# Kernel tuning notes

Measured on AMD Instinct MI355X. Metric: run time of the kernel, lower is better.

The kernel has to match this reference:

```python
import jax, jax.numpy as jnp
import numpy as np

# Qwen2 MoE MLP layer: top-k router -> token dispatch -> grouped SwiGLU MLP -> weighted combine.
S, B, H = 2048, 1, 1024      # seq, batch, hidden
E, K, F = 8, 2, 1408         # num_experts, top_k, moe_intermediate (fc1 emits 2*F for SwiGLU)

def setup_inputs() -> dict:
    key = jax.random.key(0)
    k1, k2, k3, k4 = jax.random.split(key, 4)
    return {
        "hidden_states": jax.random.normal(k1, (S, B, H), jnp.float32),
        "router_weight": jax.random.normal(k2, (H, E), jnp.float32) * 0.02,
        "w1": jax.random.normal(k3, (E, H, 2 * F), jnp.float32) * 0.02,  # grouped fc1 (gate|up)
        "w2": jax.random.normal(k4, (E, F, H), jnp.float32) * 0.02,      # grouped fc2
    }

def reference(hidden_states, router_weight, w1, w2):
    s, b, h = hidden_states.shape
    x = hidden_states.reshape(-1, h)                      # [T, H], T = S*B
    logits = x @ router_weight                            # [T, E]
    probs = jax.nn.softmax(logits, axis=-1)
    _, topk_idx = jax.lax.top_k(probs, K)                 # token -> top-k expert ids
    routing_map = jax.nn.one_hot(topk_idx, E, dtype=probs.dtype).sum(axis=1)  # [T, E] 0/1 mask
    local_probs = probs * routing_map                     # combine weights, zero off-topk
    # Grouped SwiGLU MLP. The torch module permutes tokens to expert groups and runs
    # grouped GEMMs; with static shapes the equivalent math is dense-per-expert with
    # the routing mask folded into the combine weights (identical output).
    y = jnp.einsum('th,ehf->tef', x, w1)                  # [T, E, 2F]
    y1, y2 = jnp.split(y, 2, axis=-1)
    g = jax.nn.silu(y1) * y2                              # swiglu, [T, E, F]
    o = jnp.einsum('tef,efh->teh', g, w2)                 # [T, E, H]
    out = jnp.einsum('teh,te->th', o, local_probs)        # unpermute + prob-weighted combine
    return out.reshape(s, b, h)
```

## Files before the change

### kernel.cpp

```cpp
#include <hip/hip_runtime.h>
#include <hip/hip_bf16.h>
#include <stdint.h>

#define T_TOK 2048
#define HD    1024
#define NE    8
#define FD    1408
#define F2D   2816
#define HP    1056
#define OP    1056

#define BM 128
#define BK 32
#define MAXMT 40
#define MAXSLOTS 5120
#define FC1_NT 22
#define FC2_NT 16
#define FC1_NWG (FC1_NT * MAXMT)
#define FC2_NWG (FC2_NT * MAXMT)
#define FC1_CHUNK 110
#define FC2_CHUNK 80

typedef __attribute__((ext_vector_type(8))) short bf16x8;
typedef __attribute__((ext_vector_type(4))) float f32x4;
typedef __attribute__((ext_vector_type(2))) int i32x2;

__device__ __forceinline__ unsigned short f2bf(float f) {
  unsigned int u = __float_as_uint(f);
  u += 0x7FFFu + ((u >> 16) & 1u);
  return (unsigned short)(u >> 16);
}

#define GLL16(gp, lp) __builtin_amdgcn_global_load_lds( \
    (const __attribute__((address_space(1))) void*)(gp), \
    (__attribute__((address_space(3))) void*)(lp), 16, 0, 0)

#define LDS_OFF(p) ((unsigned)(uintptr_t)(__attribute__((address_space(3))) const unsigned short*)(p))

__device__ __forceinline__ void tr_issue(unsigned a, i32x2& lo, i32x2& hi) {
  asm volatile("ds_read_b64_tr_b16 %0, %2\n\t"
               "ds_read_b64_tr_b16 %1, %2 offset:512"
               : "=&v"(lo), "=&v"(hi)
               : "v"(a)
               : "memory");
}
__device__ __forceinline__ bf16x8 tr_pack(i32x2 lo, i32x2 hi) {
  union { i32x2 v; short s[4]; } a, b;
  a.v = lo; b.v = hi;
  bf16x8 f;
  f[0] = a.s[0]; f[1] = a.s[1]; f[2] = a.s[2]; f[3] = a.s[3];
  f[4] = b.s[0]; f[5] = b.s[1]; f[6] = b.s[2]; f[7] = b.s[3];
  return f;
}

__global__ __launch_bounds__(256) void k_router(
    const float* __restrict__ x, const float* __restrict__ rw,
    unsigned short* __restrict__ xbf, int* __restrict__ ctrl,
    int* __restrict__ tok_e, float* __restrict__ tok_p)
{
  const int lane = threadIdx.x & 63;
  const int t = blockIdx.x * 4 + (threadIdx.x >> 6);
  const float* xr = x + (size_t)t * HD;

  float part[8];
#pragma unroll
  for (int e = 0; e < 8; ++e) part[e] = 0.f;

#pragma unroll
  for (int i = 0; i < 16; ++i) {
    const int h = i * 64 + lane;
    const float xv = xr[h];
    xbf[(size_t)t * HP + h] = f2bf(xv);
    const float4* rwr = reinterpret_cast<const float4*>(rw + (size_t)h * 8);
    float4 a = rwr[0], bb = rwr[1];
    part[0] += xv * a.x; part[1] += xv * a.y; part[2] += xv * a.z; part[3] += xv * a.w;
    part[4] += xv * bb.x; part[5] += xv * bb.y; part[6] += xv * bb.z; part[7] += xv * bb.w;
  }
#pragma unroll
  for (int e = 0; e < 8; ++e) {
    float v = part[e];
#pragma unroll
    for (int d = 32; d; d >>= 1) v += __shfl_xor(v, d, 64);
    part[e] = v;
  }
  float m = part[0];
#pragma unroll
  for (int e = 1; e < 8; ++e) m = fmaxf(m, part[e]);
  float p[8], s = 0.f;
#pragma unroll
  for (int e = 0; e < 8; ++e) { p[e] = __expf(part[e] - m); s += p[e]; }
  const float inv = 1.f / s;
#pragma unroll
  for (int e = 0; e < 8; ++e) p[e] *= inv;

  int e0 = 0; float p0 = p[0];
#pragma unroll
  for (int e = 1; e < 8; ++e) if (p[e] > p0) { p0 = p[e]; e0 = e; }
  int e1 = -1; float p1 = -1.f;
#pragma unroll
  for (int e = 0; e < 8; ++e) if (e != e0 && p[e] > p1) { p1 = p[e]; e1 = e; }

  if (lane == 0) {
    tok_e[t * 2 + 0] = e0; tok_e[t * 2 + 1] = e1;
    tok_p[t * 2 + 0] = p0; tok_p[t * 2 + 1] = p1;
    atomicAdd(&ctrl[e0], 1);
    atomicAdd(&ctrl[e1], 1);
  }
}

__global__ __launch_bounds__(256) void k_offsets(
    int* __restrict__ ctrl, const int* __restrict__ tok_e,
    const float* __restrict__ tok_p, int* __restrict__ stok,
    float* __restrict__ sp, int* __restrict__ tslot,
    int* __restrict__ widmt1, int* __restrict__ widmt2)
{
  __shared__ int soff[8], scnt[8], sFirst[8], sNmt[8], sTake[8], sCur[8];
  __shared__ int sSpill;
  if (threadIdx.x == 0) {
    int o = 0, nm = 0, spill = 0;
    for (int e = 0; e < 8; ++e) {
      ctrl[16 + e] = o; soff[e] = o; scnt[e] = ctrl[e]; sCur[e] = 0;
      const int n = ctrl[e];
      const int nmt = (n + BM - 1) / BM;
      sFirst[e] = nm; sNmt[e] = nmt; sTake[e] = nmt < 5 ? nmt : 5;
      if (nmt > 5) spill = 1;
      for (int j = 0; j < nmt; ++j) { ctrl[24 + nm] = e; ctrl[64 + nm] = o + j * BM; ++nm; }
      o += nmt * BM;
    }
    for (int i = nm; i < MAXMT; ++i) ctrl[24 + i] = -1;
    sSpill = spill;
  }
  __syncthreads();
  for (int i = threadIdx.x; i < FC1_NWG; i += 256) {
    const int e = i / FC1_CHUNK, r = i % FC1_CHUNK;
    const int j = r / FC1_NT, n = r % FC1_NT;
    widmt1[i] = (j < sTake[e]) ? (sFirst[e] + j) * 32 + n : -1;
  }
  for (int i = threadIdx.x; i < FC2_NWG; i += 256) {
    const int e = i / FC2_CHUNK, r = i % FC2_CHUNK;
    const int j = r / FC2_NT, n = r % FC2_NT;
    widmt2[i] = (j < sTake[e]) ? (sFirst[e] + j) * 32 + n : -1;
  }
  __syncthreads();
  if (sSpill && threadIdx.x == 0) {
    int cur = 0;
    for (int e = 0; e < 8; ++e)
      for (int j = 5; j < sNmt[e]; ++j)
        for (int n = 0; n < FC1_NT; ++n) {
          while (widmt1[cur] != -1) ++cur;
          widmt1[cur] = (sFirst[e] + j) * 32 + n;
        }
    cur = 0;
    for (int e = 0; e < 8; ++e)
      for (int j = 5; j < sNmt[e]; ++j)
        for (int n = 0; n < FC2_NT; ++n) {
          while (widmt2[cur] != -1) ++cur;
          widmt2[cur] = (sFirst[e] + j) * 32 + n;
        }
  }
  for (int e = 0; e < 8; ++e) {
    const int n = scnt[e], o = soff[e];
    const int padEnd = (n + BM - 1) / BM * BM;
    for (int j = n + (int)threadIdx.x; j < padEnd; j += 256) {
      stok[o + j] = 0; sp[o + j] = 0.f;
    }
  }
  for (int i = threadIdx.x; i < T_TOK; i += 256) {
#pragma unroll
    for (int k = 0; k < 2; ++k) {
      const int e = tok_e[i * 2 + k];
      const int pos = atomicAdd(&sCur[e], 1);
      const int slot = soff[e] + pos;
      stok[slot] = i; sp[slot] = tok_p[i * 2 + k];
      tslot[i * 2 + k] = slot;
    }
  }
}

__global__ __launch_bounds__(256) void k_fc1(
    const unsigned short* __restrict__ xbf,
    const float* __restrict__ w1,
    const int* __restrict__ ctrl,
    const int* __restrict__ stok,
    const float* __restrict__ sp,
    const int* __restrict__ widmt1,
    unsigned short* __restrict__ g)
{
  const int bid = blockIdx.x;
  const int wid = (bid & 7) * FC1_CHUNK + (bid >> 3);
  const int packed = widmt1[wid];
  if (packed < 0) return;
  const int mt = packed >> 5;
  const int e = ctrl[24 + mt];
  const int rowbase = ctrl[64 + mt];
  const int n0 = (packed & 31) * 64;

  __shared__ unsigned short sA[3][BM * BK];
  __shared__ unsigned short sB1[3][64 * BK];
  __shared__ unsigned short sB2[3][64 * BK];

  const int tid = threadIdx.x;
  const int lane = tid & 63;
  const int wave = tid >> 6;
  const int wm = wave >> 1, wn = wave & 1;

  const int schunk = (lane & 3) ^ ((lane >> 3) & 3);
  const unsigned short* aSrc[2];
#pragma unroll
  for (int t4 = 0; t4 < 2; ++t4) {
    const int row = (t4 * 4 + wave) * 16 + (lane >> 2);
    const int tok = stok[rowbase + row];
    aSrc[t4] = xbf + (size_t)tok * HP + schunk * 8;
  }

  const int kdec = wave * 8 + ((lane >> 5) << 2) + ((lane >> 1) & 3);
  const int ndec = ((lane >> 3) & 3) * 16 + (lane & 1) * 8;
  const float* b1SrcF = w1 + ((size_t)e * HD + kdec) * F2D + n0 + ndec;
  const float* b2SrcF = b1SrcF + FD;

  const int c = lane >> 4;
  int aoff[4];
#pragma unroll
  for (int m = 0; m < 4; ++m) {
    const int row = wm * 64 + m * 16 + (lane & 15);
    aoff[m] = row * 32 + ((c ^ ((row >> 1) & 3)) << 3);
  }
  const unsigned trlane = (lane & 15) * 8 + (lane >> 4) * 1024;
  unsigned trb[2];
#pragma unroll
  for (int n = 0; n < 2; ++n) trb[n] = trlane + (wn * 2 + n) * 128;
  const unsigned b1base = LDS_OFF(&sB1[0][0]);
  const unsigned b2base = LDS_OFF(&sB2[0][0]);

  const f32x4 zero = {0.f, 0.f, 0.f, 0.f};
  f32x4 acc1[4][2], acc2[4][2];
#pragma unroll
  for (int m = 0; m < 4; ++m)
#pragma unroll
    for (int n = 0; n < 2; ++n) { acc1[m][n] = zero; acc2[m][n] = zero; }

  float b1r0[8], b2r0[8], b1r1[8], b2r1[8];

#define FC1_BLOAD(KT, R1, R2) do {                                  \
    const float* _p1 = b1SrcF + (size_t)(KT) * BK * F2D;            \
    const float* _p2 = b2SrcF + (size_t)(KT) * BK * F2D;            \
    *(float4*)&R1[0] = *(const float4*)_p1;                         \
    *(float4*)&R1[4] = *(const float4*)(_p1 + 4);                   \
    *(float4*)&R2[0] = *(const float4*)_p2;                         \
    *(float4*)&R2[4] = *(const float4*)(_p2 + 4);                   \
  } while (0)

#define FC1_BWRITE(BUF, R1, R2) do {                                \
    unsigned _a0,_a1,_a2,_a3,_c0,_c1,_c2,_c3;                       \
    asm("v_cvt_pk_bf16_f32 %0, %1, %2" : "=v"(_a0) : "v"(R1[0]), "v"(R1[1])); \
    asm("v_cvt_pk_bf16_f32 %0, %1, %2" : "=v"(_a1) : "v"(R1[2]), "v"(R1[3])); \
    asm("v_cvt_pk_bf16_f32 %0, %1, %2" : "=v"(_a2) : "v"(R1[4]), "v"(R1[5])); \
    asm("v_cvt_pk_bf16_f32 %0, %1, %2" : "=v"(_a3) : "v"(R1[6]), "v"(R1[7])); \
    asm("v_cvt_pk_bf16_f32 %0, %1, %2" : "=v"(_c0) : "v"(R2[0]), "v"(R2[1])); \
    asm("v_cvt_pk_bf16_f32 %0, %1, %2" : "=v"(_c1) : "v"(R2[2]), "v"(R2[3])); \
    asm("v_cvt_pk_bf16_f32 %0, %1, %2" : "=v"(_c2) : "v"(R2[4]), "v"(R2[5])); \
    asm("v_cvt_pk_bf16_f32 %0, %1, %2" : "=v"(_c3) : "v"(R2[6]), "v"(R2[7])); \
    uint4 _u1 = make_uint4(_a0,_a1,_a2,_a3);                        \
    uint4 _u2 = make_uint4(_c0,_c1,_c2,_c3);                        \
    *(uint4*)&sB1[BUF][wave * 512 + lane * 8] = _u1;                \
    *(uint4*)&sB2[BUF][wave * 512 + lane * 8] = _u2;                \
  } while (0)

#define FC1_ASTAGE(BUF, KT) do {                                    \
    for (int _t4 = 0; _t4 < 2; ++_t4)                               \
      GLL16(aSrc[_t4] + (size_t)(KT) * BK, &sA[BUF][(_t4 * 4 + wave) * 512]); \
  } while (0)

  const int NSTEP = HD / BK;
  FC1_BLOAD(0, b1r0, b2r0);
  __builtin_amdgcn_sched_barrier(0);
  asm volatile("s_waitcnt vmcnt(0)" ::: "memory");
  FC1_BWRITE(0, b1r0, b2r0);
  __builtin_amdgcn_sched_barrier(0);
  FC1_BLOAD(1, b1r1, b2r1);
  __builtin_amdgcn_sched_barrier(0);
  FC1_ASTAGE(0, 0);
  __builtin_amdgcn_sched_barrier(0);
  FC1_BLOAD(2, b1r0, b2r0);
  __builtin_amdgcn_sched_barrier(0);
  FC1_ASTAGE(1, 1);
  __builtin_amdgcn_sched_barrier(0);
  asm volatile("s_waitcnt lgkmcnt(0)" ::: "memory");

#define FC1_STEP(T, R1, R2) do {                                             \
    const int _t = (T);                                                      \
    if (_t < NSTEP - 2)      { asm volatile("s_waitcnt vmcnt(6)" ::: "memory"); } \
    else if (_t == NSTEP - 2){ asm volatile("s_waitcnt vmcnt(2)" ::: "memory"); } \
    else                     { asm volatile("s_waitcnt vmcnt(0)" ::: "memory"); } \
    __builtin_amdgcn_s_barrier();                                            \
    __builtin_amdgcn_sched_barrier(0);                                       \
    int _bnext = bsel + 1; if (_bnext >= 3) _bnext -= 3;                     \
    int _bn2 = bsel + 2; if (_bn2 >= 3) _bn2 -= 3;                           \
    if (_t + 1 < NSTEP) FC1_BWRITE(_bnext, R1, R2);                          \
    __builtin_amdgcn_sched_barrier(0);                                       \
    if (_t + 3 < NSTEP) FC1_BLOAD(_t + 3, R1, R2);                           \
    __builtin_amdgcn_sched_barrier(0);                                       \
    if (_t + 2 < NSTEP) FC1_ASTAGE(_bn2, _t + 2);                            \
    __builtin_amdgcn_sched_barrier(0);                                       \
    bf16x8 _af[4];                                                           \
    for (int _m = 0; _m < 4; ++_m)                                           \
      _af[_m] = *(const bf16x8*)&sA[bsel][aoff[_m]];                         \
    __builtin_amdgcn_sched_barrier(0);                                       \
    i32x2 _q1lo[2], _q1hi[2], _q2lo[2], _q2hi[2];                            \
    tr_issue(b1base + bsel * 4096 + trb[0], _q1lo[0], _q1hi[0]);             \
    tr_issue(b2base + bsel * 4096 + trb[0], _q2lo[0], _q2hi[0]);             \
    __builtin_amdgcn_sched_barrier(0);                                       \
    tr_issue(b1base + bsel * 4096 + trb[1], _q1lo[1], _q1hi[1]);             \
    tr_issue(b2base + bsel * 4096 + trb[1], _q2lo[1], _q2hi[1]);             \
    asm volatile("s_waitcnt lgkmcnt(4)" ::: "memory");                       \
    __builtin_amdgcn_sched_barrier(0);                                       \
    bf16x8 _b1f0 = tr_pack(_q1lo[0], _q1hi[0]);                              \
    bf16x8 _b2f0 = tr_pack(_q2lo[0], _q2hi[0]);                              \
    __builtin_amdgcn_s_setprio(1);                                           \
    for (int _m = 0; _m < 4; ++_m) {                                         \
      acc1[_m][0] = __builtin_amdgcn_mfma_f32_16x16x32_bf16(_af[_m], _b1f0, acc1[_m][0], 0, 0, 0); \
      acc2[_m][0] = __builtin_amdgcn_mfma_f32_16x16x32_bf16(_af[_m], _b2f0, acc2[_m][0], 0, 0, 0); \
    }                                                                        \
    __builtin_amdgcn_s_setprio(0);                                           \
    asm volatile("s_waitcnt lgkmcnt(0)" ::: "memory");                       \
    __builtin_amdgcn_sched_barrier(0);                                       \
    bf16x8 _b1f1 = tr_pack(_q1lo[1], _q1hi[1]);                              \
    bf16x8 _b2f1 = tr_pack(_q2lo[1], _q2hi[1]);                              \
    __builtin_amdgcn_s_setprio(1);                                           \
    for (int _m = 0; _m < 4; ++_m) {                                         \
      acc1[_m][1] = __builtin_amdgcn_mfma_f32_16x16x32_bf16(_af[_m], _b1f1, acc1[_m][1], 0, 0, 0); \
      acc2[_m][1] = __builtin_amdgcn_mfma_f32_16x16x32_bf16(_af[_m], _b2f1, acc2[_m][1], 0, 0, 0); \
    }                                                                        \
    __builtin_amdgcn_s_setprio(0);                                           \
  } while (0)

  int bsel = 0;
  for (int tt = 0; tt < NSTEP; tt += 2) {
    FC1_STEP(tt, b1r1, b2r1);
    bsel = bsel + 1 == 3 ? 0 : bsel + 1;
    FC1_STEP(tt + 1, b1r0, b2r0);
    bsel = bsel + 1 == 3 ? 0 : bsel + 1;
  }

  float prv[4][4];
#pragma unroll
  for (int m = 0; m < 4; ++m)
#pragma unroll
    for (int r = 0; r < 4; ++r)
      prv[m][r] = sp[rowbase + wm * 64 + m * 16 + (lane >> 4) * 4 + r];

#pragma unroll
  for (int m = 0; m < 4; ++m) {
    const int rb = rowbase + wm * 64 + m * 16 + (lane >> 4) * 4;
#pragma unroll
    for (int n = 0; n < 2; ++n) {
      const int col = n0 + wn * 32 + n * 16 + (lane & 15);
#pragma unroll
      for (int r = 0; r < 4; ++r) {
        const float y1 = acc1[m][n][r];
        const float y2 = acc2[m][n][r];
        const float gv = y1 / (1.f + __expf(-y1)) * y2 * prv[m][r];
        g[(size_t)(rb + r) * FD + col] = f2bf(gv);
      }
    }
  }
}

__global__ __launch_bounds__(256) void k_fc2(
    const unsigned short* __restrict__ g,
    const float* __restrict__ w2,
    const int* __restrict__ ctrl,
    const int* __restrict__ widmt2,
    float* __restrict__ o)
{
  const int bid = blockIdx.x;
  const int wid = (bid & 7) * FC2_CHUNK + (bid >> 3);
  const int packed = widmt2[wid];
  if (packed < 0) return;
  const int mt = packed >> 5;
  const int e = ctrl[24 + mt];
  const int rowbase = ctrl[64 + mt];
  const int n0 = (packed & 31) * 64;

  __shared__ unsigned short sA[3][BM * BK];
  __shared__ unsigned short sB[3][64 * BK];

  const int tid = threadIdx.x;
  const int lane = tid & 63;
  const int wave = tid >> 6;
  const int wm = wave >> 1, wn = wave & 1;

  const int schunk = (lane & 3) ^ ((lane >> 3) & 3);
  const unsigned short* aSrc[2];
#pragma unroll
  for (int t4 = 0; t4 < 2; ++t4) {
    const int row = (t4 * 4 + wave) * 16 + (lane >> 2);
    aSrc[t4] = g + (size_t)(rowbase + row) * FD + schunk * 8;
  }

  const int kdec = wave * 8 + ((lane >> 5) << 2) + ((lane >> 1) & 3);
  const int ndec = ((lane >> 3) & 3) * 16 + (lane & 1) * 8;
  const float* bSrcF = w2 + ((size_t)e * FD + kdec) * HD + n0 + ndec;

  const int c = lane >> 4;
  int aoff[4];
#pragma unroll
  for (int m = 0; m < 4; ++m) {
    const int row = wm * 64 + m * 16 + (lane & 15);
    aoff[m] = row * 32 + ((c ^ ((row >> 1) & 3)) << 3);
  }
  const unsigned trlane = (lane & 15) * 8 + (lane >> 4) * 1024;
  unsigned trb[2];
#pragma unroll
  for (int n = 0; n < 2; ++n) trb[n] = trlane + (wn * 2 + n) * 128;
  const unsigned bbase = LDS_OFF(&sB[0][0]);

  const f32x4 zero = {0.f, 0.f, 0.f, 0.f};
  f32x4 acc[4][2];
#pragma unroll
  for (int m = 0; m < 4; ++m)
#pragma unroll
    for (int n = 0; n < 2; ++n) acc[m][n] = zero;

  float br0[8], br1[8];

#define FC2_BLOAD(KT, R) do {                                       \
    const float* _p = bSrcF + (size_t)(KT) * BK * HD;               \
    *(float4*)&R[0] = *(const float4*)_p;                           \
    *(float4*)&R[4] = *(const float4*)(_p + 4);                     \
  } while (0)

#define FC2_BWRITE(BUF, R) do {                                     \
    unsigned _a0,_a1,_a2,_a3;                                       \
    asm("v_cvt_pk_bf16_f32 %0, %1, %2" : "=v"(_a0) : "v"(R[0]), "v"(R[1])); \
    asm("v_cvt_pk_bf16_f32 %0, %1, %2" : "=v"(_a1) : "v"(R[2]), "v"(R[3])); \
    asm("v_cvt_pk_bf16_f32 %0, %1, %2" : "=v"(_a2) : "v"(R[4]), "v"(R[5])); \
    asm("v_cvt_pk_bf16_f32 %0, %1, %2" : "=v"(_a3) : "v"(R[6]), "v"(R[7])); \
    uint4 _u = make_uint4(_a0,_a1,_a2,_a3);                         \
    *(uint4*)&sB[BUF][wave * 512 + lane * 8] = _u;                  \
  } while (0)

#define FC2_ASTAGE(BUF, KT) do {                                    \
    for (int _t4 = 0; _t4 < 2; ++_t4)                               \
      GLL16(aSrc[_t4] + (size_t)(KT) * BK, &sA[BUF][(_t4 * 4 + wave) * 512]); \
  } while (0)

  const int NSTEP = FD / BK;
  FC2_BLOAD(0, br0);
  __builtin_amdgcn_sched_barrier(0);
  asm volatile("s_waitcnt vmcnt(0)" ::: "memory");
  FC2_BWRITE(0, br0);
  __builtin_amdgcn_sched_barrier(0);
  FC2_BLOAD(1, br1);
  __builtin_amdgcn_sched_barrier(0);
  FC2_ASTAGE(0, 0);
  __builtin_amdgcn_sched_barrier(0);
  FC2_BLOAD(2, br0);
  __builtin_amdgcn_sched_barrier(0);
  FC2_ASTAGE(1, 1);
  __builtin_amdgcn_sched_barrier(0);
  asm volatile("s_waitcnt lgkmcnt(0)" ::: "memory");

#define FC2_STEP(T, R) do {                                                  \
    const int _t = (T);                                                      \
    if (_t < NSTEP - 2)      { asm volatile("s_waitcnt vmcnt(4)" ::: "memory"); } \
    else if (_t == NSTEP - 2){ asm volatile("s_waitcnt vmcnt(2)" ::: "memory"); } \
    else                     { asm volatile("s_waitcnt vmcnt(0)" ::: "memory"); } \
    __builtin_amdgcn_s_barrier();                                            \
    __builtin_amdgcn_sched_barrier(0);                                       \
    int _bnext = bsel + 1; if (_bnext >= 3) _bnext -= 3;                     \
    int _bn2 = bsel + 2; if (_bn2 >= 3) _bn2 -= 3;                           \
    if (_t + 1 < NSTEP) FC2_BWRITE(_bnext, R);                               \
    __builtin_amdgcn_sched_barrier(0);                                       \
    if (_t + 3 < NSTEP) FC2_BLOAD(_t + 3, R);                                \
    __builtin_amdgcn_sched_barrier(0);                                       \
    if (_t + 2 < NSTEP) FC2_ASTAGE(_bn2, _t + 2);                            \
    __builtin_amdgcn_sched_barrier(0);                                       \
    bf16x8 _af[4];                                                           \
    for (int _m = 0; _m < 4; ++_m)                                           \
      _af[_m] = *(const bf16x8*)&sA[bsel][aoff[_m]];                         \
    __builtin_amdgcn_sched_barrier(0);                                       \
    i32x2 _qlo[2], _qhi[2];                                                  \
    tr_issue(bbase + bsel * 4096 + trb[0], _qlo[0], _qhi[0]);                \
    __builtin_amdgcn_sched_barrier(0);                                       \
    tr_issue(bbase + bsel * 4096 + trb[1], _qlo[1], _qhi[1]);                \
    asm volatile("s_waitcnt lgkmcnt(2)" ::: "memory");                       \
    __builtin_amdgcn_sched_barrier(0);                                       \
    bf16x8 _bf0 = tr_pack(_qlo[0], _qhi[0]);                                 \
    __builtin_amdgcn_s_setprio(1);                                           \
    for (int _m = 0; _m < 4; ++_m)                                           \
      acc[_m][0] = __builtin_amdgcn_mfma_f32_16x16x32_bf16(_af[_m], _bf0, acc[_m][0], 0, 0, 0); \
    __builtin_amdgcn_s_setprio(0);                                           \
    asm volatile("s_waitcnt lgkmcnt(0)" ::: "memory");                       \
    __builtin_amdgcn_sched_barrier(0);                                       \
    bf16x8 _bf1 = tr_pack(_qlo[1], _qhi[1]);                                 \
    __builtin_amdgcn_s_setprio(1);                                           \
    for (int _m = 0; _m < 4; ++_m)                                           \
      acc[_m][1] = __builtin_amdgcn_mfma_f32_16x16x32_bf16(_af[_m], _bf1, acc[_m][1], 0, 0, 0); \
    __builtin_amdgcn_s_setprio(0);                                           \
  } while (0)

  int bsel = 0;
  for (int tt = 0; tt < NSTEP; tt += 2) {
    FC2_STEP(tt, br1);
    bsel = bsel + 1 == 3 ? 0 : bsel + 1;
    FC2_STEP(tt + 1, br0);
    bsel = bsel + 1 == 3 ? 0 : bsel + 1;
  }

#pragma unroll
  for (int m = 0; m < 4; ++m) {
    const int rb = rowbase + wm * 64 + m * 16 + (lane >> 4) * 4;
#pragma unroll
    for (int n = 0; n < 2; ++n) {
      const int col = n0 + wn * 32 + n * 16 + (lane & 15);
#pragma unroll
      for (int r = 0; r < 4; ++r)
        o[(size_t)(rb + r) * OP + col] = acc[m][n][r];
    }
  }
}

__global__ __launch_bounds__(256) void k_combine(
    const float* __restrict__ o, const int* __restrict__ tslot,
    float* __restrict__ out)
{
  const int t = blockIdx.x;
  const int c4 = threadIdx.x;
  const int sA = tslot[t * 2], sB = tslot[t * 2 + 1];
  const float4 a = reinterpret_cast<const float4*>(o + (size_t)sA * OP)[c4];
  const float4 b = reinterpret_cast<const float4*>(o + (size_t)sB * OP)[c4];
  float4 r;
  r.x = a.x + b.x; r.y = a.y + b.y; r.z = a.z + b.z; r.w = a.w + b.w;
  reinterpret_cast<float4*>(out)[(size_t)t * 256 + c4] = r;
}

extern "C" void kernel_launch(void* const* d_in, const int* in_sizes, int n_in,
                              void* d_out, int out_size, void* d_ws, size_t ws_size,
                              hipStream_t stream)
{
  const float* x  = (const float*)d_in[0];
  const float* rw = (const float*)d_in[1];
  const float* w1 = (const float*)d_in[2];
  const float* w2 = (const float*)d_in[3];
  float* out = (float*)d_out;
  char* ws = (char*)d_ws;

  int*   ctrl   = (int*)(ws + 0);
  int*   tok_e  = (int*)(ws + 1024);
  float* tok_p  = (float*)(ws + 17408);
  int*   stok   = (int*)(ws + 33792);
  float* sp     = (float*)(ws + 54272);
  int*   tslot  = (int*)(ws + 74752);
  int*   widmt1 = (int*)(ws + 91136);
  int*   widmt2 = (int*)(ws + 94656);
  unsigned short* xbf = (unsigned short*)(ws + 97280);
  unsigned short* g   = (unsigned short*)(ws + 4422656);
  float*          o   = (float*)(ws + 18840576);

  hipMemsetAsync(ws, 0, 1024, stream);

  k_router<<<T_TOK / 4, 256, 0, stream>>>(x, rw, xbf, ctrl, tok_e, tok_p);
  k_offsets<<<1, 256, 0, stream>>>(ctrl, tok_e, tok_p, stok, sp, tslot, widmt1, widmt2);
  k_fc1<<<FC1_NWG, 256, 0, stream>>>(xbf, w1, ctrl, stok, sp, widmt1, g);
  k_fc2<<<FC2_NWG, 256, 0, stream>>>(g, w2, ctrl, widmt2, o);
  k_combine<<<T_TOK, 256, 0, stream>>>(o, tslot, out);
}
```

Measured before the change: 170.7 us.

## Switch FC1/FC2 shared-memory pipeline from triple to double buffering for occupancy

Reduces the LDS staging for the A (activations) and B (weights) tiles in both grouped GEMM kernels from three buffers to two. The A-tile async load is now issued only one step ahead instead of two, and the vmcnt waits are tightened to match. It also adds a minimum-blocks-per-CU hint of 5 to the launch bounds. The goal is higher occupancy from the smaller LDS footprint and register cap, at the cost of less prefetch depth, so global-load latency is more exposed per step.

```diff
diff --git a/kernel.cpp b/kernel.cpp
--- a/kernel.cpp
+++ b/kernel.cpp
@@ -177,7 +177,7 @@
   }
 }
 
-__global__ __launch_bounds__(256) void k_fc1(
+__global__ __launch_bounds__(256, 5) void k_fc1(
     const unsigned short* __restrict__ xbf,
     const float* __restrict__ w1,
     const int* __restrict__ ctrl,
@@ -195,9 +195,9 @@
   const int rowbase = ctrl[64 + mt];
   const int n0 = (packed & 31) * 64;
 
-  __shared__ unsigned short sA[3][BM * BK];
-  __shared__ unsigned short sB1[3][64 * BK];
-  __shared__ unsigned short sB2[3][64 * BK];
+  __shared__ unsigned short sA[2][BM * BK];
+  __shared__ unsigned short sB1[2][64 * BK];
+  __shared__ unsigned short sB2[2][64 * BK];
 
   const int tid = threadIdx.x;
   const int lane = tid & 63;
@@ -283,35 +283,32 @@
   __builtin_amdgcn_sched_barrier(0);
   FC1_BLOAD(2, b1r0, b2r0);
   __builtin_amdgcn_sched_barrier(0);
-  FC1_ASTAGE(1, 1);
-  __builtin_amdgcn_sched_barrier(0);
   asm volatile("s_waitcnt lgkmcnt(0)" ::: "memory");
 
 #define FC1_STEP(T, R1, R2) do {                                             \
     const int _t = (T);                                                      \
-    if (_t < NSTEP - 2)      { asm volatile("s_waitcnt vmcnt(6)" ::: "memory"); } \
-    else if (_t == NSTEP - 2){ asm volatile("s_waitcnt vmcnt(2)" ::: "memory"); } \
-    else                     { asm volatile("s_waitcnt vmcnt(0)" ::: "memory"); } \
+    if (_t < NSTEP - 2) { asm volatile("s_waitcnt vmcnt(4)" ::: "memory"); } \
+    else                { asm volatile("s_waitcnt vmcnt(0)" ::: "memory"); } \
     __builtin_amdgcn_s_barrier();                                            \
     __builtin_amdgcn_sched_barrier(0);                                       \
-    int _bnext = bsel + 1; if (_bnext >= 3) _bnext -= 3;                     \
-    int _bn2 = bsel + 2; if (_bn2 >= 3) _bn2 -= 3;                           \
-    if (_t + 1 < NSTEP) FC1_BWRITE(_bnext, R1, R2);                          \
+    const int _cb = _t & 1;                                                  \
+    const int _nb = _cb ^ 1;                                                 \
+    if (_t + 1 < NSTEP) FC1_BWRITE(_nb, R1, R2);                             \
+    __builtin_amdgcn_sched_barrier(0);                                       \
+    if (_t + 1 < NSTEP) FC1_ASTAGE(_nb, _t + 1);                             \
     __builtin_amdgcn_sched_barrier(0);                                       \
     if (_t + 3 < NSTEP) FC1_BLOAD(_t + 3, R1, R2);                           \
-    __builtin_amdgcn_sched_barrier(0);                                       \
-    if (_t + 2 < NSTEP) FC1_ASTAGE(_bn2, _t + 2);                            \
     __builtin_amdgcn_sched_barrier(0);                                       \
     bf16x8 _af[4];                                                           \
     for (int _m = 0; _m < 4; ++_m)                                           \
-      _af[_m] = *(const bf16x8*)&sA[bsel][aoff[_m]];                         \
+      _af[_m] = *(const bf16x8*)&sA[_cb][aoff[_m]];                          \
     __builtin_amdgcn_sched_barrier(0);                                       \
     i32x2 _q1lo[2], _q1hi[2], _q2lo[2], _q2hi[2];                            \
-    tr_issue(b1base + bsel * 4096 + trb[0], _q1lo[0], _q1hi[0]);             \
-    tr_issue(b2base + bsel * 4096 + trb[0], _q2lo[0], _q2hi[0]);             \
-    __builtin_amdgcn_sched_barrier(0);                                       \
-    tr_issue(b1base + bsel * 4096 + trb[1], _q1lo[1], _q1hi[1]);             \
-    tr_issue(b2base + bsel * 4096 + trb[1], _q2lo[1], _q2hi[1]);             \
+    tr_issue(b1base + _cb * 4096 + trb[0], _q1lo[0], _q1hi[0]);              \
+    tr_issue(b2base + _cb * 4096 + trb[0], _q2lo[0], _q2hi[0]);              \
+    __builtin_amdgcn_sched_barrier(0);                                       \
+    tr_issue(b1base + _cb * 4096 + trb[1], _q1lo[1], _q1hi[1]);              \
+    tr_issue(b2base + _cb * 4096 + trb[1], _q2lo[1], _q2hi[1]);              \
     asm volatile("s_waitcnt lgkmcnt(4)" ::: "memory");                       \
     __builtin_amdgcn_sched_barrier(0);                                       \
     bf16x8 _b1f0 = tr_pack(_q1lo[0], _q1hi[0]);                              \
@@ -334,12 +331,9 @@
     __builtin_amdgcn_s_setprio(0);                                           \
   } while (0)
 
-  int bsel = 0;
   for (int tt = 0; tt < NSTEP; tt += 2) {
     FC1_STEP(tt, b1r1, b2r1);
-    bsel = bsel + 1 == 3 ? 0 : bsel + 1;
     FC1_STEP(tt + 1, b1r0, b2r0);
-    bsel = bsel + 1 == 3 ? 0 : bsel + 1;
   }
 
   float prv[4][4];
@@ -366,7 +360,7 @@
   }
 }
 
-__global__ __launch_bounds__(256) void k_fc2(
+__global__ __launch_bounds__(256, 5) void k_fc2(
     const unsigned short* __restrict__ g,
     const float* __restrict__ w2,
     const int* __restrict__ ctrl,
@@ -382,8 +376,8 @@
   const int rowbase = ctrl[64 + mt];
   const int n0 = (packed & 31) * 64;
 
-  __shared__ unsigned short sA[3][BM * BK];
-  __shared__ unsigned short sB[3][64 * BK];
+  __shared__ unsigned short sA[2][BM * BK];
+  __shared__ unsigned short sB[2][64 * BK];
 
   const int tid = threadIdx.x;
   const int lane = tid & 63;
@@ -457,33 +451,30 @@
   __builtin_amdgcn_sched_barrier(0);
   FC2_BLOAD(2, br0);
   __builtin_amdgcn_sched_barrier(0);
-  FC2_ASTAGE(1, 1);
-  __builtin_amdgcn_sched_barrier(0);
   asm volatile("s_waitcnt lgkmcnt(0)" ::: "memory");
 
 #define FC2_STEP(T, R) do {                                                  \
     const int _t = (T);                                                      \
-    if (_t < NSTEP - 2)      { asm volatile("s_waitcnt vmcnt(4)" ::: "memory"); } \
-    else if (_t == NSTEP - 2){ asm volatile("s_waitcnt vmcnt(2)" ::: "memory"); } \
-    else                     { asm volatile("s_waitcnt vmcnt(0)" ::: "memory"); } \
+    if (_t < NSTEP - 2) { asm volatile("s_waitcnt vmcnt(2)" ::: "memory"); } \
+    else                { asm volatile("s_waitcnt vmcnt(0)" ::: "memory"); } \
     __builtin_amdgcn_s_barrier();                                            \
     __builtin_amdgcn_sched_barrier(0);                                       \
-    int _bnext = bsel + 1; if (_bnext >= 3) _bnext -= 3;                     \
-    int _bn2 = bsel + 2; if (_bn2 >= 3) _bn2 -= 3;                           \
-    if (_t + 1 < NSTEP) FC2_BWRITE(_bnext, R);                               \
+    const int _cb = _t & 1;                                                  \
+    const int _nb = _cb ^ 1;                                                 \
+    if (_t + 1 < NSTEP) FC2_BWRITE(_nb, R);                                  \
+    __builtin_amdgcn_sched_barrier(0);                                       \
+    if (_t + 1 < NSTEP) FC2_ASTAGE(_nb, _t + 1);                             \
     __builtin_amdgcn_sched_barrier(0);                                       \
     if (_t + 3 < NSTEP) FC2_BLOAD(_t + 3, R);                                \
-    __builtin_amdgcn_sched_barrier(0);                                       \
-    if (_t + 2 < NSTEP) FC2_ASTAGE(_bn2, _t + 2);                            \
     __builtin_amdgcn_sched_barrier(0);                                       \
     bf16x8 _af[4];                                                           \
     for (int _m = 0; _m < 4; ++_m)                                           \
-      _af[_m] = *(const bf16x8*)&sA[bsel][aoff[_m]];                         \
+      _af[_m] = *(const bf16x8*)&sA[_cb][aoff[_m]];                          \
     __builtin_amdgcn_sched_barrier(0);                                       \
     i32x2 _qlo[2], _qhi[2];                                                  \
-    tr_issue(bbase + bsel * 4096 + trb[0], _qlo[0], _qhi[0]);                \
-    __builtin_amdgcn_sched_barrier(0);                                       \
-    tr_issue(bbase + bsel * 4096 + trb[1], _qlo[1], _qhi[1]);                \
+    tr_issue(bbase + _cb * 4096 + trb[0], _qlo[0], _qhi[0]);                 \
+    __builtin_amdgcn_sched_barrier(0);                                       \
+    tr_issue(bbase + _cb * 4096 + trb[1], _qlo[1], _qhi[1]);                 \
     asm volatile("s_waitcnt lgkmcnt(2)" ::: "memory");                       \
     __builtin_amdgcn_sched_barrier(0);                                       \
     bf16x8 _bf0 = tr_pack(_qlo[0], _qhi[0]);                                 \
@@ -500,12 +491,9 @@
     __builtin_amdgcn_s_setprio(0);                                           \
   } while (0)
 
-  int bsel = 0;
   for (int tt = 0; tt < NSTEP; tt += 2) {
     FC2_STEP(tt, br1);
-    bsel = bsel + 1 == 3 ? 0 : bsel + 1;
     FC2_STEP(tt + 1, br0);
-    bsel = bsel + 1 == 3 ? 0 : bsel + 1;
   }
 
 #pragma unroll
```

After: 460.6 us. +169.7%, slower.
